# Performance work log

Measured on AMD Instinct MI355X. Metric: run time of the kernel, lower is better.

Reference implementation:

```python
import jax, jax.numpy as jnp
import numpy as np

B, T, IN, H, L, V = 64, 196, 512, 512, 2, 5000


def _uniform(key, shape, bound):
    return jax.random.uniform(key, shape, jnp.float32, -bound, bound)


def setup_inputs() -> dict:
    key = jax.random.key(0)
    ks = jax.random.split(key, 16)
    bound = 1.0 / np.sqrt(H)  # PyTorch LSTM/Linear init range
    inp = {"x": jax.random.normal(ks[0], (B, 512, 14, 14), jnp.float32)}
    ki = 1
    for l in range(L):
        in_dim = IN if l == 0 else H
        inp[f"W_ih{l}"] = _uniform(ks[ki], (4 * H, in_dim), bound); ki += 1
        inp[f"W_hh{l}"] = _uniform(ks[ki], (4 * H, H), bound); ki += 1
        inp[f"b_ih{l}"] = _uniform(ks[ki], (4 * H,), bound); ki += 1
        inp[f"b_hh{l}"] = _uniform(ks[ki], (4 * H,), bound); ki += 1
    inp["W_fc"] = _uniform(ks[ki], (V, H), bound); ki += 1
    inp["b_fc"] = _uniform(ks[ki], (V,), bound)
    return inp


def lstm_layer(x, W_ih, W_hh, b_ih, b_hh):
    """Single PyTorch-convention LSTM layer. x: (B, T, in_dim) -> (B, T, H).
    Gate order: input, forget, cell(g), output."""
    Bx = x.shape[0]
    Hh = W_hh.shape[1]
    # Precompute input projection for all timesteps in one GEMM: (B, T, 4H)
    xp = jnp.einsum('bti,gi->btg', x, W_ih) + b_ih + b_hh

    def step(carry, xt):
        h, c = carry
        g = xt + h @ W_hh.T  # (B, 4H)
        i, f, gg, o = jnp.split(g, 4, axis=-1)
        i = jax.nn.sigmoid(i)
        f = jax.nn.sigmoid(f)
        gg = jnp.tanh(gg)
        o = jax.nn.sigmoid(o)
        c = f * c + i * gg
        h = o * jnp.tanh(c)
        return (h, c), h

    h0 = jnp.zeros((Bx, Hh), x.dtype)
    _, hs = jax.lax.scan(step, (h0, h0), jnp.swapaxes(xp, 0, 1))  # (T, B, H)
    return jnp.swapaxes(hs, 0, 1)


def reference(x, W_ih0, W_hh0, b_ih0, b_hh0, W_ih1, W_hh1, b_ih1, b_hh1, W_fc, b_fc):
    bsz = x.shape[0]
    seq = x.reshape(bsz, 512, 14 * 14).transpose(0, 2, 1)  # (B, 196, 512)
    h = lstm_layer(seq, W_ih0, W_hh0, b_ih0, b_hh0)
    h = lstm_layer(h, W_ih1, W_hh1, b_ih1, b_hh1)
    return jnp.einsum('bth,vh->btv', h, W_fc) + b_fc  # (B, 196, V)
```

## Files before the change

### kernel.cpp

```cpp
#include <hip/hip_runtime.h>
#include <hip/hip_bf16.h>
#include <stdint.h>

typedef unsigned short ushort_t;
typedef __bf16 bf16x8 __attribute__((ext_vector_type(8)));
typedef float f32x4 __attribute__((ext_vector_type(4)));

#define T_STEPS 196

#define O_WPACK 0u
#define SZ_WPACK (2u*2048u*1024u*2u)
#define O_WFC   (O_WPACK + SZ_WPACK)
#define SZ_WFC  (5120u*512u*2u)
#define O_BIAS  (O_WFC + SZ_WFC)
#define SZ_BIAS (2u*2048u*4u)
#define O_SEQT  (O_BIAS + SZ_BIAS)
#define SZ_SEQT (196u*64u*512u*2u)
#define O_H     (O_SEQT + SZ_SEQT)
#define SZ_H    (2u*196u*64u*512u*2u)
#define O_FLG   (O_H + SZ_H)
#define N_FLG   256u

#define SCAN_LDS_BYTES (64*1032*2 + 16*520*2 + 64*16*4)

__device__ __forceinline__ ushort_t f2bf(float v) {
  __hip_bfloat16 h = __float2bfloat16(v);
  return __builtin_bit_cast(ushort_t, h);
}

__device__ __forceinline__ void poll32(unsigned int* f, unsigned int tgt, int lane) {
  int n = 0;
  for (;;) {
    unsigned int v = __hip_atomic_load(&f[lane & 31], __ATOMIC_RELAXED,
                                       __HIP_MEMORY_SCOPE_AGENT);
    if (__all((int)(v >= tgt))) break;
    if (++n > (1 << 22)) break;
  }
  asm volatile("" ::: "memory");
}

__global__ __launch_bounds__(256) void prep_pack(
    const float* __restrict__ Wih0, const float* __restrict__ Whh0,
    const float* __restrict__ bih0, const float* __restrict__ bhh0,
    const float* __restrict__ Wih1, const float* __restrict__ Whh1,
    const float* __restrict__ bih1, const float* __restrict__ bhh1,
    const float* __restrict__ Wfc,
    ushort_t* __restrict__ wpack, ushort_t* __restrict__ wfcp,
    float* __restrict__ bias, unsigned int* __restrict__ flg)
{
  const size_t NW_ = 2u*2048u*1024u;
  const size_t NF  = 5120u*512u;
  const size_t NB  = 2u*2048u;
  const size_t TOT = NW_ + NF + NB + N_FLG;
  for (size_t idx = (size_t)blockIdx.x*256 + threadIdx.x; idx < TOT;
       idx += (size_t)gridDim.x*256) {
    if (idx < NW_) {
      int l   = (int)(idx >> 21);
      int rem = (int)(idx & ((1u<<21)-1));
      int r = rem >> 10, k = rem & 1023;
      const float* src = (k < 512) ? (l ? Wih1 : Wih0) : (l ? Whh1 : Whh0);
      wpack[idx] = f2bf(src[(size_t)r*512 + (k & 511)]);
    } else if (idx < NW_ + NF) {
      size_t i2 = idx - NW_;
      int n = (int)(i2 >> 9), k = (int)(i2 & 511);
      wfcp[i2] = (n < 5000) ? f2bf(Wfc[(size_t)n*512 + k]) : (ushort_t)0;
    } else if (idx < NW_ + NF + NB) {
      size_t i2 = idx - NW_ - NF;
      int l = (int)(i2 >> 11), r = (int)(i2 & 2047);
      bias[i2] = l ? (bih1[r] + bhh1[r]) : (bih0[r] + bhh0[r]);
    } else {
      flg[idx - NW_ - NF - NB] = 0u;
    }
  }
}

__global__ __launch_bounds__(256) void prep_seq(const float* __restrict__ x,
                                                ushort_t* __restrict__ seqT)
{
  __shared__ float tile[64 * 197];
  int b = blockIdx.x >> 3, ic = blockIdx.x & 7;
  const float* src = x + ((size_t)b*512 + ic*64) * 196;
  for (int it = 0; it < 49; ++it) {
    int idx = threadIdx.x + it*256;
    int row = idx / 196, t = idx % 196;
    tile[row*197 + t] = src[idx];
  }
  __syncthreads();
  for (int it = 0; it < 49; ++it) {
    int idx = threadIdx.x + it*256;
    int t = idx >> 6, ii = idx & 63;
    seqT[(size_t)t*(64*512) + (size_t)b*512 + ic*64 + ii] = f2bf(tile[ii*197 + t]);
  }
}

__global__ __launch_bounds__(256, 1) void lstm_scan(
    const ushort_t* __restrict__ wpack, const float* __restrict__ bias,
    const ushort_t* __restrict__ seqT, ushort_t* __restrict__ h_all,
    unsigned int* flags)
{
  extern __shared__ char smem[];
  ushort_t* w_s  = (ushort_t*)smem;
  ushort_t* in_s = (ushort_t*)(smem + 64*1032*2);
  float*    g_s  = (float*)(smem + 64*1032*2 + 16*520*2);

  const int wg = blockIdx.x;
  const int layer = wg >> 7;
  const int bs = (wg >> 5) & 3;
  const int gs = wg & 31;
  const int tid = threadIdx.x;
  const int wv = tid >> 6;
  const int lane = tid & 63;
  const int lr = lane & 15;
  const int lg = lane >> 4;

  const ushort_t* wbase = wpack + (size_t)layer * (2048*1024);
  #pragma unroll 4
  for (int it = 0; it < 32; ++it) {
    int ch = tid + it*256;
    int row = ch >> 7, kc = ch & 127;
    int q = row >> 4, j = row & 15;
    const ushort_t* g = wbase + (size_t)(512*q + gs*16 + j)*1024 + kc*8;
    *(uint4*)&w_s[row*1032 + kc*8] = *(const uint4*)g;
  }

  unsigned int* flg_self = flags + (layer*4 + bs)*32;
  unsigned int* flg_dep  = flags + bs*32;

  const int b_loc = tid >> 4;
  const int hd    = tid & 15;
  const float b_i = bias[layer*2048 +    0 + gs*16 + hd];
  const float b_f = bias[layer*2048 +  512 + gs*16 + hd];
  const float b_g = bias[layer*2048 + 1024 + gs*16 + hd];
  const float b_o = bias[layer*2048 + 1536 + gs*16 + hd];

  ushort_t* hout = h_all + (size_t)layer * (196*64*512);
  const ushort_t* hdep = h_all;

  float c_reg = 0.f;
  const int wrow = (wv*16 + lr) * 1032;
  const int brow = lr * 520;
  const int koff = lg * 8;

  for (int t = 0; t < T_STEPS; ++t) {
    if (layer == 1) {
      if (wv == 0) poll32(flg_dep, (unsigned)(t + 1), lane);
      __syncthreads();
      const ushort_t* xsrc = hdep + ((size_t)t*64 + bs*16) * 512;
      #pragma unroll
      for (int it = 0; it < 8; ++it) {
        int ch = tid + it*256;
        int row = ch >> 7, kc = ch & 127;
        unsigned long long v = __hip_atomic_load(
            (unsigned long long*)&xsrc[row*512 + kc*4],
            __ATOMIC_RELAXED, __HIP_MEMORY_SCOPE_AGENT);
        *(unsigned long long*)&in_s[row*520 + kc*4] = v;
      }
    } else {
      const ushort_t* xsrc = seqT + ((size_t)t*64 + bs*16) * 512;
      #pragma unroll
      for (int it = 0; it < 4; ++it) {
        int ch = tid + it*256;
        int row = ch >> 6, kc = ch & 63;
        *(uint4*)&in_s[row*520 + kc*8] = *(const uint4*)&xsrc[row*512 + kc*8];
      }
    }
    __syncthreads();

    f32x4 acc = {0.f, 0.f, 0.f, 0.f};
    #pragma unroll
    for (int ks = 0; ks < 16; ++ks) {
      bf16x8 a = *(const bf16x8*)&w_s[wrow + ks*32 + koff];
      bf16x8 bb = *(const bf16x8*)&in_s[brow + ks*32 + koff];
      acc = __builtin_amdgcn_mfma_f32_16x16x32_bf16(a, bb, acc, 0, 0, 0);
    }

    if (t > 0) {
      if (wv == 0) poll32(flg_self, (unsigned)t, lane);
      __syncthreads();
      const ushort_t* hsrc = hout + ((size_t)(t-1)*64 + bs*16) * 512;
      #pragma unroll
      for (int it = 0; it < 8; ++it) {
        int ch = tid + it*256;
        int row = ch >> 7, kc = ch & 127;
        unsigned long long v = __hip_atomic_load(
            (unsigned long long*)&hsrc[row*512 + kc*4],
            __ATOMIC_RELAXED, __HIP_MEMORY_SCOPE_AGENT);
        *(unsigned long long*)&in_s[row*520 + kc*4] = v;
      }
      __syncthreads();
      #pragma unroll
      for (int ks = 0; ks < 16; ++ks) {
        bf16x8 a = *(const bf16x8*)&w_s[wrow + 512 + ks*32 + koff];
        bf16x8 bb = *(const bf16x8*)&in_s[brow + ks*32 + koff];
        acc = __builtin_amdgcn_mfma_f32_16x16x32_bf16(a, bb, acc, 0, 0, 0);
      }
    }

    #pragma unroll
    for (int j2 = 0; j2 < 4; ++j2)
      g_s[(wv*16 + lg*4 + j2)*16 + lr] = acc[j2];
    __syncthreads();

    float gi = g_s[(  0 + hd)*16 + b_loc] + b_i;
    float gf = g_s[( 16 + hd)*16 + b_loc] + b_f;
    float gg = g_s[( 32 + hd)*16 + b_loc] + b_g;
    float go = g_s[( 48 + hd)*16 + b_loc] + b_o;
    float si = 1.f/(1.f + __expf(-gi));
    float sf = 1.f/(1.f + __expf(-gf));
    float tg = tanhf(gg);
    float so = 1.f/(1.f + __expf(-go));
    c_reg = sf*c_reg + si*tg;
    float hv = so * tanhf(c_reg);

    unsigned int hb = (unsigned int)f2bf(hv);
    unsigned int other = __shfl_xor(hb, 1);
    if ((tid & 1) == 0) {
      unsigned int packed = hb | (other << 16);
      __hip_atomic_store(
          (unsigned int*)&hout[((size_t)t*64 + bs*16 + b_loc)*512 + gs*16 + hd],
          packed, __ATOMIC_RELAXED, __HIP_MEMORY_SCOPE_AGENT);
    }

    __syncthreads();
    if (tid == 0)
      __hip_atomic_store(&flg_self[gs], (unsigned)(t + 1),
                         __ATOMIC_RELAXED, __HIP_MEMORY_SCOPE_AGENT);
  }
}

__global__ __launch_bounds__(256, 2) void fc_gemm(
    const ushort_t* __restrict__ h1,
    const ushort_t* __restrict__ wfc,
    const float* __restrict__ bfc,
    float* __restrict__ out)
{
  __shared__ ushort_t As[128*32];
  __shared__ ushort_t Bs[128*32];
  const int tid = threadIdx.x;
  const int wvid = tid >> 6, lane = tid & 63;
  const int lr = lane & 15, lg = lane >> 4;
  const int wr = wvid >> 1, wc = wvid & 1;
  const int m0 = blockIdx.x * 128, n0 = blockIdx.y * 128;

  f32x4 acc[4][4];
  #pragma unroll
  for (int i = 0; i < 4; ++i)
    #pragma unroll
    for (int j = 0; j < 4; ++j)
      acc[i][j] = (f32x4){0.f, 0.f, 0.f, 0.f};

  for (int kt = 0; kt < 16; ++kt) {
    #pragma unroll
    for (int c = 0; c < 2; ++c) {
      int chb = wvid*128 + c*64;
      int ch = chb + lane;
      int m = ch >> 2, kh = ch & 3;
      const ushort_t* ga = h1  + (size_t)(m0 + m)*512 + kt*32 + kh*8;
      __builtin_amdgcn_global_load_lds(
          (const __attribute__((address_space(1))) void*)ga,
          (__attribute__((address_space(3))) void*)&As[chb*8], 16, 0, 0);
      const ushort_t* gb = wfc + (size_t)(n0 + m)*512 + kt*32 + kh*8;
      __builtin_amdgcn_global_load_lds(
          (const __attribute__((address_space(1))) void*)gb,
          (__attribute__((address_space(3))) void*)&Bs[chb*8], 16, 0, 0);
    }
    asm volatile("s_waitcnt vmcnt(0)" ::: "memory");
    __syncthreads();

    bf16x8 af[4], bf_[4];
    #pragma unroll
    for (int i = 0; i < 4; ++i)
      af[i] = *(const bf16x8*)&As[(wr*64 + i*16 + lr)*32 + lg*8];
    #pragma unroll
    for (int j = 0; j < 4; ++j)
      bf_[j] = *(const bf16x8*)&Bs[(wc*64 + j*16 + lr)*32 + lg*8];
    #pragma unroll
    for (int i = 0; i < 4; ++i)
      #pragma unroll
      for (int j = 0; j < 4; ++j)
        acc[i][j] = __builtin_amdgcn_mfma_f32_16x16x32_bf16(af[i], bf_[j], acc[i][j], 0, 0, 0);
    __syncthreads();
  }

  #pragma unroll
  for (int j = 0; j < 4; ++j) {
    int coln = n0 + wc*64 + j*16 + lr;
    if (coln >= 5000) continue;
    float bb = bfc[coln];
    #pragma unroll
    for (int i = 0; i < 4; ++i) {
      #pragma unroll
      for (int jj = 0; jj < 4; ++jj) {
        int rowm = m0 + wr*64 + i*16 + lg*4 + jj;
        int tt = rowm >> 6, b2 = rowm & 63;
        out[(size_t)b2*980000 + (size_t)tt*5000 + coln] = acc[i][j][jj] + bb;
      }
    }
  }
}

extern "C" void kernel_launch(void* const* d_in, const int* in_sizes, int n_in,
                              void* d_out, int out_size, void* d_ws, size_t ws_size,
                              hipStream_t stream) {
  const float* x    = (const float*)d_in[0];
  const float* Wih0 = (const float*)d_in[1];
  const float* Whh0 = (const float*)d_in[2];
  const float* bih0 = (const float*)d_in[3];
  const float* bhh0 = (const float*)d_in[4];
  const float* Wih1 = (const float*)d_in[5];
  const float* Whh1 = (const float*)d_in[6];
  const float* bih1 = (const float*)d_in[7];
  const float* bhh1 = (const float*)d_in[8];
  const float* Wfc  = (const float*)d_in[9];
  const float* bfc  = (const float*)d_in[10];

  char* ws = (char*)d_ws;
  ushort_t* wpack = (ushort_t*)(ws + O_WPACK);
  ushort_t* wfcp  = (ushort_t*)(ws + O_WFC);
  float*    bias  = (float*)(ws + O_BIAS);
  ushort_t* seqT  = (ushort_t*)(ws + O_SEQT);
  ushort_t* h_all = (ushort_t*)(ws + O_H);
  unsigned int* flags = (unsigned int*)(ws + O_FLG);

  hipFuncSetAttribute((const void*)lstm_scan,
                      hipFuncAttributeMaxDynamicSharedMemorySize, SCAN_LDS_BYTES);

  prep_pack<<<4096, 256, 0, stream>>>(Wih0, Whh0, bih0, bhh0,
                                      Wih1, Whh1, bih1, bhh1,
                                      Wfc, wpack, wfcp, bias, flags);
  prep_seq<<<512, 256, 0, stream>>>(x, seqT);
  lstm_scan<<<256, 256, SCAN_LDS_BYTES, stream>>>(wpack, bias, seqT, h_all, flags);
  dim3 fcg(98, 40);
  fc_gemm<<<fcg, 256, 0, stream>>>(h_all + (size_t)196*64*512, wfcp, bfc,
                                   (float*)d_out);
}
```

Before: 1.491 ms.

## Replace flag polling with sentinel-valued h buffers and precompute layer-0 input projection

Removes the per-step flag counters and instead fills the hidden-state buffer with 0xFF sentinels, so consumers spin directly on the data until no sentinel remains. The layer-0 input projection (plus bias) is hoisted into a separate bf16 MFMA GEMM whose output is staged in the output buffer, so the recurrent loop only does the h·W_hh part for layer 0. Layer 1 prefetches its own previous h into registers while waiting on layer 0. It also uses split accumulators, a padded gate scratch layout and cheaper rcp-based sigmoid/tanh. The tradeoffs are an extra memset and GEMM launch, and a reliance on a bf16 0xFFFF pair (a NaN) never appearing as a real hidden value.

```diff
diff --git a/kernel.cpp b/kernel.cpp
--- a/kernel.cpp
+++ b/kernel.cpp
@@ -5,6 +5,7 @@
 typedef unsigned short ushort_t;
 typedef __bf16 bf16x8 __attribute__((ext_vector_type(8)));
 typedef float f32x4 __attribute__((ext_vector_type(4)));
+typedef unsigned long long u64;
 
 #define T_STEPS 196
 
@@ -18,25 +19,25 @@
 #define SZ_SEQT (196u*64u*512u*2u)
 #define O_H     (O_SEQT + SZ_SEQT)
 #define SZ_H    (2u*196u*64u*512u*2u)
-#define O_FLG   (O_H + SZ_H)
-#define N_FLG   256u
-
-#define SCAN_LDS_BYTES (64*1032*2 + 16*520*2 + 64*16*4)
+
+
+#define SCAN_LDS_BYTES (64*1032*2 + 16*520*2 + 64*17*4)
 
 __device__ __forceinline__ ushort_t f2bf(float v) {
   __hip_bfloat16 h = __float2bfloat16(v);
   return __builtin_bit_cast(ushort_t, h);
 }
-
-__device__ __forceinline__ void poll32(unsigned int* f, unsigned int tgt, int lane) {
-  int n = 0;
-  for (;;) {
-    unsigned int v = __hip_atomic_load(&f[lane & 31], __ATOMIC_RELAXED,
-                                       __HIP_MEMORY_SCOPE_AGENT);
-    if (__all((int)(v >= tgt))) break;
-    if (++n > (1 << 22)) break;
-  }
-  asm volatile("" ::: "memory");
+__device__ __forceinline__ u64 ald64(const void* p) {
+  return __hip_atomic_load((const u64*)p, __ATOMIC_RELAXED, __HIP_MEMORY_SCOPE_AGENT);
+}
+__device__ __forceinline__ bool valid64(u64 v) {
+  return ((unsigned)v != 0xFFFFFFFFu) && ((unsigned)(v >> 32) != 0xFFFFFFFFu);
+}
+__device__ __forceinline__ float sigm(float x) {
+  return __builtin_amdgcn_rcpf(1.f + __expf(-x));
+}
+__device__ __forceinline__ float tanh_f(float x) {
+  return 1.f - 2.f * __builtin_amdgcn_rcpf(1.f + __expf(2.f * x));
 }
 
 __global__ __launch_bounds__(256) void prep_pack(
@@ -46,12 +47,12 @@
     const float* __restrict__ bih1, const float* __restrict__ bhh1,
     const float* __restrict__ Wfc,
     ushort_t* __restrict__ wpack, ushort_t* __restrict__ wfcp,
-    float* __restrict__ bias, unsigned int* __restrict__ flg)
+    float* __restrict__ bias)
 {
   const size_t NW_ = 2u*2048u*1024u;
   const size_t NF  = 5120u*512u;
   const size_t NB  = 2u*2048u;
-  const size_t TOT = NW_ + NF + NB + N_FLG;
+  const size_t TOT = NW_ + NF + NB;
   for (size_t idx = (size_t)blockIdx.x*256 + threadIdx.x; idx < TOT;
        idx += (size_t)gridDim.x*256) {
     if (idx < NW_) {
@@ -64,12 +65,10 @@
       size_t i2 = idx - NW_;
       int n = (int)(i2 >> 9), k = (int)(i2 & 511);
       wfcp[i2] = (n < 5000) ? f2bf(Wfc[(size_t)n*512 + k]) : (ushort_t)0;
-    } else if (idx < NW_ + NF + NB) {
+    } else {
       size_t i2 = idx - NW_ - NF;
       int l = (int)(i2 >> 11), r = (int)(i2 & 2047);
       bias[i2] = l ? (bih1[r] + bhh1[r]) : (bih0[r] + bhh0[r]);
-    } else {
-      flg[idx - NW_ - NF - NB] = 0u;
     }
   }
 }
@@ -93,10 +92,79 @@
   }
 }
 
+__global__ __launch_bounds__(256, 2) void xp_gemm(
+    const ushort_t* __restrict__ wih,
+    const ushort_t* __restrict__ xseq,
+    const float* __restrict__ bias,
+    float* __restrict__ xp)
+{
+  __shared__ ushort_t As[128*32];
+  __shared__ ushort_t Bs[128*32];
+  const int tid = threadIdx.x;
+  const int wvid = tid >> 6, lane = tid & 63;
+  const int lr = lane & 15, lg = lane >> 4;
+  const int wr = wvid >> 1, wc = wvid & 1;
+  const int m0 = blockIdx.x * 128, n0 = blockIdx.y * 128;
+
+  f32x4 acc[4][4];
+  #pragma unroll
+  for (int i = 0; i < 4; ++i)
+    #pragma unroll
+    for (int j = 0; j < 4; ++j)
+      acc[i][j] = (f32x4){0.f, 0.f, 0.f, 0.f};
+
+  for (int kt = 0; kt < 16; ++kt) {
+    #pragma unroll
+    for (int c = 0; c < 2; ++c) {
+      int chb = wvid*128 + c*64;
+      int ch = chb + lane;
+      int m = ch >> 2, kh = ch & 3;
+      const ushort_t* ga = wih + (size_t)(m0 + m)*1024 + kt*32 + kh*8;
+      __builtin_amdgcn_global_load_lds(
+          (const __attribute__((address_space(1))) void*)ga,
+          (__attribute__((address_space(3))) void*)&As[chb*8], 16, 0, 0);
+      const ushort_t* gb = xseq + (size_t)(n0 + m)*512 + kt*32 + kh*8;
+      __builtin_amdgcn_global_load_lds(
+          (const __attribute__((address_space(1))) void*)gb,
+          (__attribute__((address_space(3))) void*)&Bs[chb*8], 16, 0, 0);
+    }
+    asm volatile("s_waitcnt vmcnt(0)" ::: "memory");
+    __syncthreads();
+
+    bf16x8 af[4], bf_[4];
+    #pragma unroll
+    for (int i = 0; i < 4; ++i)
+      af[i] = *(const bf16x8*)&As[(wr*64 + i*16 + lr)*32 + lg*8];
+    #pragma unroll
+    for (int j = 0; j < 4; ++j)
+      bf_[j] = *(const bf16x8*)&Bs[(wc*64 + j*16 + lr)*32 + lg*8];
+    #pragma unroll
+    for (int i = 0; i < 4; ++i)
+      #pragma unroll
+      for (int j = 0; j < 4; ++j)
+        acc[i][j] = __builtin_amdgcn_mfma_f32_16x16x32_bf16(af[i], bf_[j], acc[i][j], 0, 0, 0);
+    __syncthreads();
+  }
+
+  #pragma unroll
+  for (int i = 0; i < 4; ++i) {
+    int g0 = m0 + wr*64 + i*16 + lg*4;
+    f32x4 b4 = *(const f32x4*)&bias[g0];
+    int q = g0 >> 9, u = g0 & 511;
+    int gsl = u >> 4, j0 = u & 15;
+    #pragma unroll
+    for (int j = 0; j < 4; ++j) {
+      int n = n0 + wc*64 + j*16 + lr;
+      int t = n >> 6, b = n & 63;
+      size_t idx = (((size_t)t*4 + (b>>4))*32 + gsl)*1024 + (size_t)(b&15)*64 + q*16 + j0;
+      *(f32x4*)&xp[idx] = acc[i][j] + b4;
+    }
+  }
+}
+
 __global__ __launch_bounds__(256, 1) void lstm_scan(
     const ushort_t* __restrict__ wpack, const float* __restrict__ bias,
-    const ushort_t* __restrict__ seqT, ushort_t* __restrict__ h_all,
-    unsigned int* flags)
+    ushort_t* __restrict__ h_all, const float* __restrict__ xp)
 {
   extern __shared__ char smem[];
   ushort_t* w_s  = (ushort_t*)smem;
@@ -114,17 +182,21 @@
   const int lg = lane >> 4;
 
   const ushort_t* wbase = wpack + (size_t)layer * (2048*1024);
-  #pragma unroll 4
-  for (int it = 0; it < 32; ++it) {
-    int ch = tid + it*256;
-    int row = ch >> 7, kc = ch & 127;
-    int q = row >> 4, j = row & 15;
-    const ushort_t* g = wbase + (size_t)(512*q + gs*16 + j)*1024 + kc*8;
-    *(uint4*)&w_s[row*1032 + kc*8] = *(const uint4*)g;
-  }
-
-  unsigned int* flg_self = flags + (layer*4 + bs)*32;
-  unsigned int* flg_dep  = flags + bs*32;
+  if (layer == 0) {
+    for (int ch = tid; ch < 4096; ch += 256) {
+      int row = ch >> 6, kc = 64 + (ch & 63);
+      int q = row >> 4, j = row & 15;
+      const ushort_t* g = wbase + (size_t)(512*q + gs*16 + j)*1024 + kc*8;
+      *(uint4*)&w_s[row*1032 + kc*8] = *(const uint4*)g;
+    }
+  } else {
+    for (int ch = tid; ch < 8192; ch += 256) {
+      int row = ch >> 7, kc = ch & 127;
+      int q = row >> 4, j = row & 15;
+      const ushort_t* g = wbase + (size_t)(512*q + gs*16 + j)*1024 + kc*8;
+      *(uint4*)&w_s[row*1032 + kc*8] = *(const uint4*)g;
+    }
+  }
 
   const int b_loc = tid >> 4;
   const int hd    = tid & 15;
@@ -140,77 +212,140 @@
   const int wrow = (wv*16 + lr) * 1032;
   const int brow = lr * 520;
   const int koff = lg * 8;
+  const float* xq = xp + ((size_t)bs*32 + gs)*1024 + (size_t)lr*64 + wv*16 + lg*4;
 
   for (int t = 0; t < T_STEPS; ++t) {
-    if (layer == 1) {
-      if (wv == 0) poll32(flg_dep, (unsigned)(t + 1), lane);
+    f32x4 acc_a = {0.f,0.f,0.f,0.f}, acc_b = {0.f,0.f,0.f,0.f};
+
+    if (layer == 0) {
+      acc_a = *(const f32x4*)&xq[(size_t)t*131072];
+      if (t > 0) {
+        const ushort_t* hsrc = hout + ((size_t)(t-1)*64 + bs*16) * 512;
+        u64 v[8];
+        int guard = 200000;
+        for (;;) {
+          #pragma unroll
+          for (int it = 0; it < 8; ++it) {
+            int ch = tid + it*256; int row = ch >> 7, kc = ch & 127;
+            v[it] = ald64(&hsrc[row*512 + kc*4]);
+          }
+          bool ok = true;
+          #pragma unroll
+          for (int it = 0; it < 8; ++it) ok &= valid64(v[it]);
+          if (ok || --guard == 0) break;
+        }
+        #pragma unroll
+        for (int it = 0; it < 8; ++it) {
+          int ch = tid + it*256; int row = ch >> 7, kc = ch & 127;
+          *(u64*)&in_s[row*520 + kc*4] = v[it];
+        }
+      }
       __syncthreads();
-      const ushort_t* xsrc = hdep + ((size_t)t*64 + bs*16) * 512;
-      #pragma unroll
-      for (int it = 0; it < 8; ++it) {
-        int ch = tid + it*256;
-        int row = ch >> 7, kc = ch & 127;
-        unsigned long long v = __hip_atomic_load(
-            (unsigned long long*)&xsrc[row*512 + kc*4],
-            __ATOMIC_RELAXED, __HIP_MEMORY_SCOPE_AGENT);
-        *(unsigned long long*)&in_s[row*520 + kc*4] = v;
+      if (t > 0) {
+        #pragma unroll
+        for (int ks = 0; ks < 8; ++ks) {
+          bf16x8 a = *(const bf16x8*)&w_s[wrow + 512 + ks*32 + koff];
+          bf16x8 bb = *(const bf16x8*)&in_s[brow + ks*32 + koff];
+          acc_a = __builtin_amdgcn_mfma_f32_16x16x32_bf16(a, bb, acc_a, 0, 0, 0);
+        }
+        #pragma unroll
+        for (int ks = 8; ks < 16; ++ks) {
+          bf16x8 a = *(const bf16x8*)&w_s[wrow + 512 + ks*32 + koff];
+          bf16x8 bb = *(const bf16x8*)&in_s[brow + ks*32 + koff];
+          acc_b = __builtin_amdgcn_mfma_f32_16x16x32_bf16(a, bb, acc_b, 0, 0, 0);
+        }
       }
     } else {
-      const ushort_t* xsrc = seqT + ((size_t)t*64 + bs*16) * 512;
-      #pragma unroll
-      for (int it = 0; it < 4; ++it) {
-        int ch = tid + it*256;
-        int row = ch >> 6, kc = ch & 63;
-        *(uint4*)&in_s[row*520 + kc*8] = *(const uint4*)&xsrc[row*512 + kc*8];
-      }
-    }
-    __syncthreads();
-
-    f32x4 acc = {0.f, 0.f, 0.f, 0.f};
-    #pragma unroll
-    for (int ks = 0; ks < 16; ++ks) {
-      bf16x8 a = *(const bf16x8*)&w_s[wrow + ks*32 + koff];
-      bf16x8 bb = *(const bf16x8*)&in_s[brow + ks*32 + koff];
-      acc = __builtin_amdgcn_mfma_f32_16x16x32_bf16(a, bb, acc, 0, 0, 0);
-    }
-
-    if (t > 0) {
-      if (wv == 0) poll32(flg_self, (unsigned)t, lane);
-      __syncthreads();
-      const ushort_t* hsrc = hout + ((size_t)(t-1)*64 + bs*16) * 512;
-      #pragma unroll
-      for (int it = 0; it < 8; ++it) {
-        int ch = tid + it*256;
-        int row = ch >> 7, kc = ch & 127;
-        unsigned long long v = __hip_atomic_load(
-            (unsigned long long*)&hsrc[row*512 + kc*4],
-            __ATOMIC_RELAXED, __HIP_MEMORY_SCOPE_AGENT);
-        *(unsigned long long*)&in_s[row*520 + kc*4] = v;
+      u64 f0[16], f1[16];
+      const ushort_t* hp = hout + ((size_t)(t-1)*64 + bs*16) * 512;
+      if (t > 0) {
+        #pragma unroll
+        for (int ks = 0; ks < 16; ++ks) {
+          f0[ks] = ald64(&hp[lr*512 + ks*32 + lg*8]);
+          f1[ks] = ald64(&hp[lr*512 + ks*32 + lg*8 + 4]);
+        }
+      }
+      {
+        const ushort_t* xsrc = hdep + ((size_t)t*64 + bs*16) * 512;
+        u64 v[8];
+        int guard = 200000;
+        for (;;) {
+          #pragma unroll
+          for (int it = 0; it < 8; ++it) {
+            int ch = tid + it*256; int row = ch >> 7, kc = ch & 127;
+            v[it] = ald64(&xsrc[row*512 + kc*4]);
+          }
+          bool ok = true;
+          #pragma unroll
+          for (int it = 0; it < 8; ++it) ok &= valid64(v[it]);
+          if (ok || --guard == 0) break;
+        }
+        #pragma unroll
+        for (int it = 0; it < 8; ++it) {
+          int ch = tid + it*256; int row = ch >> 7, kc = ch & 127;
+          *(u64*)&in_s[row*520 + kc*4] = v[it];
+        }
       }
       __syncthreads();
       #pragma unroll
-      for (int ks = 0; ks < 16; ++ks) {
-        bf16x8 a = *(const bf16x8*)&w_s[wrow + 512 + ks*32 + koff];
+      for (int ks = 0; ks < 8; ++ks) {
+        bf16x8 a = *(const bf16x8*)&w_s[wrow + ks*32 + koff];
         bf16x8 bb = *(const bf16x8*)&in_s[brow + ks*32 + koff];
-        acc = __builtin_amdgcn_mfma_f32_16x16x32_bf16(a, bb, acc, 0, 0, 0);
-      }
-    }
-
+        acc_a = __builtin_amdgcn_mfma_f32_16x16x32_bf16(a, bb, acc_a, 0, 0, 0);
+      }
+      #pragma unroll
+      for (int ks = 8; ks < 16; ++ks) {
+        bf16x8 a = *(const bf16x8*)&w_s[wrow + ks*32 + koff];
+        bf16x8 bb = *(const bf16x8*)&in_s[brow + ks*32 + koff];
+        acc_b = __builtin_amdgcn_mfma_f32_16x16x32_bf16(a, bb, acc_b, 0, 0, 0);
+      }
+      if (t > 0) {
+        int guard = 200000;
+        for (;;) {
+          bool ok = true;
+          #pragma unroll
+          for (int ks = 0; ks < 16; ++ks) ok &= valid64(f0[ks]) && valid64(f1[ks]);
+          if (ok || --guard == 0) break;
+          #pragma unroll
+          for (int ks = 0; ks < 16; ++ks) {
+            f0[ks] = ald64(&hp[lr*512 + ks*32 + lg*8]);
+            f1[ks] = ald64(&hp[lr*512 + ks*32 + lg*8 + 4]);
+          }
+        }
+        #pragma unroll
+        for (int ks = 0; ks < 8; ++ks) {
+          bf16x8 a = *(const bf16x8*)&w_s[wrow + 512 + ks*32 + koff];
+          ulonglong2 p; p.x = f0[ks]; p.y = f1[ks];
+          bf16x8 bb = __builtin_bit_cast(bf16x8, p);
+          acc_a = __builtin_amdgcn_mfma_f32_16x16x32_bf16(a, bb, acc_a, 0, 0, 0);
+        }
+        #pragma unroll
+        for (int ks = 8; ks < 16; ++ks) {
+          bf16x8 a = *(const bf16x8*)&w_s[wrow + 512 + ks*32 + koff];
+          ulonglong2 p; p.x = f0[ks]; p.y = f1[ks];
+          bf16x8 bb = __builtin_bit_cast(bf16x8, p);
+          acc_b = __builtin_amdgcn_mfma_f32_16x16x32_bf16(a, bb, acc_b, 0, 0, 0);
+        }
+      }
+    }
+
+    f32x4 accf = acc_a + acc_b;
     #pragma unroll
     for (int j2 = 0; j2 < 4; ++j2)
-      g_s[(wv*16 + lg*4 + j2)*16 + lr] = acc[j2];
+      g_s[(wv*16 + lg*4 + j2)*17 + lr] = accf[j2];
     __syncthreads();
 
-    float gi = g_s[(  0 + hd)*16 + b_loc] + b_i;
-    float gf = g_s[( 16 + hd)*16 + b_loc] + b_f;
-    float gg = g_s[( 32 + hd)*16 + b_loc] + b_g;
-    float go = g_s[( 48 + hd)*16 + b_loc] + b_o;
-    float si = 1.f/(1.f + __expf(-gi));
-    float sf = 1.f/(1.f + __expf(-gf));
-    float tg = tanhf(gg);
-    float so = 1.f/(1.f + __expf(-go));
+    float gi = g_s[(  0 + hd)*17 + b_loc];
+    float gf = g_s[( 16 + hd)*17 + b_loc];
+    float gg = g_s[( 32 + hd)*17 + b_loc];
+    float go = g_s[( 48 + hd)*17 + b_loc];
+    if (layer == 1) { gi += b_i; gf += b_f; gg += b_g; go += b_o; }
+    float si = sigm(gi);
+    float sf = sigm(gf);
+    float tg = tanh_f(gg);
+    float so = sigm(go);
     c_reg = sf*c_reg + si*tg;
-    float hv = so * tanhf(c_reg);
+    float hv = so * tanh_f(c_reg);
 
     unsigned int hb = (unsigned int)f2bf(hv);
     unsigned int other = __shfl_xor(hb, 1);
@@ -220,11 +355,6 @@
           (unsigned int*)&hout[((size_t)t*64 + bs*16 + b_loc)*512 + gs*16 + hd],
           packed, __ATOMIC_RELAXED, __HIP_MEMORY_SCOPE_AGENT);
     }
-
-    __syncthreads();
-    if (tid == 0)
-      __hip_atomic_store(&flg_self[gs], (unsigned)(t + 1),
-                         __ATOMIC_RELAXED, __HIP_MEMORY_SCOPE_AGENT);
   }
 }
 
@@ -320,16 +450,18 @@
   float*    bias  = (float*)(ws + O_BIAS);
   ushort_t* seqT  = (ushort_t*)(ws + O_SEQT);
   ushort_t* h_all = (ushort_t*)(ws + O_H);
-  unsigned int* flags = (unsigned int*)(ws + O_FLG);
+  float*    xp    = (float*)d_out;
 
   hipFuncSetAttribute((const void*)lstm_scan,
                       hipFuncAttributeMaxDynamicSharedMemorySize, SCAN_LDS_BYTES);
 
   prep_pack<<<4096, 256, 0, stream>>>(Wih0, Whh0, bih0, bhh0,
                                       Wih1, Whh1, bih1, bhh1,
-                                      Wfc, wpack, wfcp, bias, flags);
+                                      Wfc, wpack, wfcp, bias);
   prep_seq<<<512, 256, 0, stream>>>(x, seqT);
-  lstm_scan<<<256, 256, SCAN_LDS_BYTES, stream>>>(wpack, bias, seqT, h_all, flags);
+  hipMemsetAsync(h_all, 0xFF, SZ_H, stream);
+  xp_gemm<<<dim3(16, 98), 256, 0, stream>>>(wpack, seqT, bias, xp);
+  lstm_scan<<<256, 256, SCAN_LDS_BYTES, stream>>>(wpack, bias, h_all, xp);
   dim3 fcg(98, 40);
   fc_gemm<<<fcg, 256, 0, stream>>>(h_all + (size_t)196*64*512, wfcp, bfc,
                                    (float*)d_out);
```

Result: slower. 2.113 ms (+41.7%).
